# Performance work log

Measured on AMD Instinct MI355X. Metric: run time of the kernel, lower is better.

## Reference

```python
import jax, jax.numpy as jnp
import numpy as np

N, IN_DIM, OUT_DIM, HEADS = 2048, 512, 512, 8
HEAD_DIM = OUT_DIM // HEADS
NEG_SLOPE = 0.2


def setup_inputs() -> dict:
    key = jax.random.key(0)
    k1, k2, k3, k4 = jax.random.split(key, 4)
    x = jax.random.normal(k1, (N, IN_DIM), dtype=jnp.float32)
    adj = jax.random.randint(k2, (N, N), 0, 2, dtype=jnp.int32)
    W = jax.random.normal(k3, (IN_DIM, OUT_DIM), dtype=jnp.float32) * 0.02
    a = jax.random.normal(k4, (2 * HEAD_DIM,), dtype=jnp.float32) * 0.02
    return {"x": x, "adj": adj, "W": W, "a": a}


def reference(x, adj, W, a):
    # Wh: (N, H, Dh)
    Wh = (x @ W).reshape(N, HEADS, HEAD_DIM)
    # a . concat(Wh_i, Wh_j) == (Wh_i . a_src) + (Wh_j . a_dst) -- exact decomposition,
    # avoids materializing the (N, N, H, 2*Dh) concat tensor.
    a_src, a_dst = a[:HEAD_DIM], a[HEAD_DIM:]
    s_i = jnp.einsum('nhd,d->nh', Wh, a_src)  # contribution of dest node i
    s_j = jnp.einsum('nhd,d->nh', Wh, a_dst)  # contribution of source node j
    e = jax.nn.leaky_relu(s_i[:, None, :] + s_j[None, :, :], negative_slope=NEG_SLOPE)  # (N, N, H)
    mask = (adj > 0)[:, :, None]
    e = jnp.where(mask, e, jnp.float32(-jnp.inf))
    alpha = jax.nn.softmax(e, axis=1)  # softmax over source nodes j
    # out[i,h,:] = sum_j alpha[i,j,h] * Wh[j,h,:]   (dropout is identity at eval)
    out = jnp.einsum('ijh,jhd->ihd', alpha, Wh)
    return out.reshape(N, OUT_DIM)
```

## Files before the change

### kernel.cpp

```cpp
#include <hip/hip_runtime.h>
#include <hip/hip_bf16.h>

#define NN 2048
#define KD 512
#define ODIM 512
#define NHEAD 8
#define HD 64
#define NEG 0.2f

typedef float f32x4 __attribute__((ext_vector_type(4)));
typedef short bf16x8 __attribute__((ext_vector_type(8)));
typedef short bf16x4 __attribute__((ext_vector_type(4)));
typedef unsigned long long u64;
typedef unsigned int u32;

__device__ __forceinline__ short tob(float f) {
  __hip_bfloat16 h = __float2bfloat16(f);
  return *reinterpret_cast<short*>(&h);
}

__device__ __forceinline__ void gl_lds16(const void* g, void* l) {
  __builtin_amdgcn_global_load_lds(
      (const __attribute__((address_space(1))) u32*)g,
      (__attribute__((address_space(3))) u32*)l, 16, 0, 0);
}

__global__ __launch_bounds__(256) void prep(const float* __restrict__ W,
                                            const int* __restrict__ adj,
                                            __hip_bfloat16* __restrict__ WTb,
                                            unsigned short* __restrict__ bits) {
  const int b = blockIdx.x;
  const int t = threadIdx.x;
  if (b >= 64) {
    const int T = (b - 64) * 256 + t;
    const int row = T >> 7, g = T & 127;
    const int* p = adj + (size_t)row * NN + g * 16;
    u32 m = 0;
#pragma unroll
    for (int q = 0; q < 4; ++q) {
      const int4 v = *(const int4*)&p[q * 4];
      m |= (v.x > 0 ? 1u : 0u) << (q * 4);
      m |= (v.y > 0 ? 2u : 0u) << (q * 4);
      m |= (v.z > 0 ? 4u : 0u) << (q * 4);
      m |= (v.w > 0 ? 8u : 0u) << (q * 4);
    }
    bits[T] = (unsigned short)m;
    return;
  }
  __shared__ float tile[64][68];
  const int k0 = (b & 7) * 64, od0 = (b >> 3) * 64;
#pragma unroll
  for (int r = 0; r < 4; ++r) {
    const int flat = r * 256 + t;
    const int kk = flat >> 4, oq = (flat & 15) * 4;
    const float4 v = *(const float4*)&W[(size_t)(k0 + kk) * ODIM + od0 + oq];
    tile[kk][oq] = v.x;
    tile[kk][oq + 1] = v.y;
    tile[kk][oq + 2] = v.z;
    tile[kk][oq + 3] = v.w;
  }
  __syncthreads();
#pragma unroll
  for (int r = 0; r < 2; ++r) {
    const int flat = r * 256 + t;
    const int od = flat >> 3, kq = (flat & 7) * 8;
    bf16x8 o;
#pragma unroll
    for (int u = 0; u < 8; ++u) o[u] = tob(tile[kq + u][od]);
    *(bf16x8*)&WTb[(size_t)(od0 + od) * KD + k0 + kq] = o;
  }
}

__global__ __launch_bounds__(256) void gemm_fused(
    const float* __restrict__ X, const __hip_bfloat16* __restrict__ WTb,
    const float* __restrict__ a, short* __restrict__ WhF,
    float2* __restrict__ esrcp, u32* __restrict__ edstp) {
  __shared__ short As[64][72];
  __shared__ short Bs[64][72];
  const int t = threadIdx.x;
  const int lane = t & 63, w = t >> 6;
  const int col = lane & 15, kgrp = lane >> 4;
  const int bm = blockIdx.x * 64;
  const int h = blockIdx.y;

  const int am = t >> 2, ak = (t & 3) * 16;
  const int bn = t >> 2, bk = (t & 3) * 16;

  float4 xa[4];
  bf16x8 wb[2];
#pragma unroll
  for (int q = 0; q < 4; ++q)
    xa[q] = *(const float4*)&X[(size_t)(bm + am) * KD + ak + q * 4];
#pragma unroll
  for (int q = 0; q < 2; ++q)
    wb[q] = *(const bf16x8*)&WTb[(size_t)(h * 64 + bn) * KD + bk + q * 8];

  f32x4 acc[4] = {};

  for (int k0 = 0; k0 < KD; k0 += 64) {
#pragma unroll
    for (int q = 0; q < 2; ++q) {
      bf16x8 o;
#pragma unroll
      for (int u = 0; u < 4; ++u) {
        o[u] = tob(((const float*)&xa[q * 2])[u]);
        o[u + 4] = tob(((const float*)&xa[q * 2 + 1])[u]);
      }
      *(bf16x8*)&As[am][ak + q * 8] = o;
      *(bf16x8*)&Bs[bn][bk + q * 8] = wb[q];
    }
    __syncthreads();
    if (k0 + 64 < KD) {
      const int k1 = k0 + 64;
#pragma unroll
      for (int q = 0; q < 4; ++q)
        xa[q] = *(const float4*)&X[(size_t)(bm + am) * KD + k1 + ak + q * 4];
#pragma unroll
      for (int q = 0; q < 2; ++q)
        wb[q] = *(const bf16x8*)&WTb[(size_t)(h * 64 + bn) * KD + k1 + bk + q * 8];
    }
#pragma unroll
    for (int ks = 0; ks < 2; ++ks) {
      const bf16x8 af = *(const bf16x8*)&As[w * 16 + col][ks * 32 + kgrp * 8];
#pragma unroll
      for (int nt = 0; nt < 4; ++nt) {
        const bf16x8 bf = *(const bf16x8*)&Bs[nt * 16 + col][ks * 32 + kgrp * 8];
        acc[nt] = __builtin_amdgcn_mfma_f32_16x16x32_bf16(af, bf, acc[nt], 0, 0, 0);
      }
    }
    __syncthreads();
  }

  float asv[4], adv[4];
#pragma unroll
  for (int nt = 0; nt < 4; ++nt) {
    asv[nt] = a[nt * 16 + col];
    adv[nt] = a[64 + nt * 16 + col];
  }
  float ps[4], pd[4];
#pragma unroll
  for (int r = 0; r < 4; ++r) {
    float s1 = 0.f, s2 = 0.f;
#pragma unroll
    for (int nt = 0; nt < 4; ++nt) {
      s1 += acc[nt][r] * asv[nt];
      s2 += acc[nt][r] * adv[nt];
    }
    ps[r] = s1;
    pd[r] = s2;
  }
#pragma unroll
  for (int off = 1; off <= 8; off <<= 1) {
#pragma unroll
    for (int r = 0; r < 4; ++r) {
      ps[r] += __shfl_xor(ps[r], off);
      pd[r] += __shfl_xor(pd[r], off);
    }
  }
  {
    const size_t tbase = ((size_t)h * 32 + blockIdx.x) * 4096;
    const int lp = ((w & 1) * 2 + (kgrp >> 1)) * 16 + col;
    const int u0 = (kgrp & 1) * 4;
    const int slot_ks = w >> 1;
#pragma unroll
    for (int nt = 0; nt < 4; ++nt) {
      bf16x4 o;
#pragma unroll
      for (int r = 0; r < 4; ++r) o[r] = tob(acc[nt][r]);
      *(bf16x4*)&WhF[tbase + (size_t)(nt * 2 + slot_ks) * 512 + lp * 8 + u0] = o;
    }
  }
  if (col == 0) {
    const int mbase = bm + w * 16 + kgrp * 4;
#pragma unroll
    for (int r = 0; r < 4; ++r) {
      const int n = mbase + r;
      esrcp[h * NN + n] = make_float2(__expf(ps[r]), __expf(NEG * ps[r]));
      const u32 lo = (u32)(unsigned short)tob(__expf(pd[r]));
      const u32 hi = (u32)(unsigned short)tob(__expf(NEG * pd[r]));
      edstp[h * NN + n] = (hi << 16) | lo;
    }
  }
}

__global__ __launch_bounds__(512) void attn_mfma(
    const short* __restrict__ WhF, const unsigned char* __restrict__ adjbits,
    const float2* __restrict__ esrcp, const u32* __restrict__ edstp,
    float* __restrict__ out) {
  extern __shared__ __align__(16) char smem[];
  short* stage = (short*)smem;
  float* red = (float*)smem;

  const int t = threadIdx.x;
  const int lane = t & 63;
  const int wid = t >> 6;
  const int jq = wid >> 1;
  const int mh = wid & 1;
  const int col = lane & 15, kgrp = lane >> 4;
  const int h = blockIdx.y;
  const int i0 = blockIdx.x * 64;
  const int ib = i0 + mh * 32;

  const float2 e0 = esrcp[h * NN + ib + col];
  const float2 e1 = esrcp[h * NN + ib + 16 + col];
  const float A0 = e0.x, C0 = e0.y, A1 = e1.x, C1 = e1.y;
  const unsigned char* ab0 = adjbits + (size_t)(ib + col) * (NN / 8);
  const unsigned char* ab1 = adjbits + (size_t)(ib + 16 + col) * (NN / 8);

  bf16x8 ones;
#pragma unroll
  for (int u = 0; u < 8; ++u) ones[u] = (short)0x3F80;

  f32x4 acc[2][4] = {};
  f32x4 accd[2] = {};

  const short* tb = WhF + ((size_t)h * 32 + jq * 8) * 4096;
  const int jb = jq * 512;
  short* st0 = stage + (size_t)jq * (2 * 8 * 512);

#pragma unroll
  for (int s = 0; s < 4; ++s) {
    const int slot = mh * 4 + s;
    gl_lds16(tb + slot * 512 + lane * 8, st0 + slot * 512);
  }
  uint4 bd0, bd1, bd2, bd3;
  u64 aw0, aw1;
  {
    const int jj0 = jb + kgrp * 8;
    bd0 = *(const uint4*)&edstp[h * NN + jj0];
    bd1 = *(const uint4*)&edstp[h * NN + jj0 + 4];
    bd2 = *(const uint4*)&edstp[h * NN + jj0 + 32];
    bd3 = *(const uint4*)&edstp[h * NN + jj0 + 36];
    aw0 = *(const u64*)(ab0 + (jb >> 3));
    aw1 = *(const u64*)(ab1 + (jb >> 3));
  }
  __syncthreads();

#pragma unroll
  for (int tt = 0; tt < 8; ++tt) {
    short* scur = st0 + (tt & 1) * (8 * 512);
    short* snxt = st0 + ((tt + 1) & 1) * (8 * 512);
    if (tt < 7) {
      const short* g = tb + (size_t)(tt + 1) * 4096;
#pragma unroll
      for (int s = 0; s < 4; ++s) {
        const int slot = mh * 4 + s;
        gl_lds16(g + slot * 512 + lane * 8, snxt + slot * 512);
      }
    }
    uint4 bn0, bn1, bn2, bn3;
    u64 an0 = 0, an1 = 0;
    if (tt < 7) {
      const int j1 = jb + (tt + 1) * 64;
      const int jj1 = j1 + kgrp * 8;
      bn0 = *(const uint4*)&edstp[h * NN + jj1];
      bn1 = *(const uint4*)&edstp[h * NN + jj1 + 4];
      bn2 = *(const uint4*)&edstp[h * NN + jj1 + 32];
      bn3 = *(const uint4*)&edstp[h * NN + jj1 + 36];
      an0 = *(const u64*)(ab0 + (j1 >> 3));
      an1 = *(const u64*)(ab1 + (j1 >> 3));
    }
    bf16x8 af0[2], af1[2];
#pragma unroll
    for (int ks = 0; ks < 2; ++ks) {
      const u32 mb0 = (u32)(aw0 >> ((ks * 4 + kgrp) * 8)) & 0xffu;
      const u32 mb1 = (u32)(aw1 >> ((ks * 4 + kgrp) * 8)) & 0xffu;
      const uint4 q0 = ks ? bd2 : bd0;
      const uint4 q1 = ks ? bd3 : bd1;
      const u32 uw[8] = {q0.x, q0.y, q0.z, q0.w, q1.x, q1.y, q1.z, q1.w};
#pragma unroll
      for (int u2 = 0; u2 < 8; ++u2) {
        const float B = __uint_as_float(uw[u2] << 16);
        const float D = __uint_as_float(uw[u2] & 0xffff0000u);
        float p0 = fmaxf(A0 * B, C0 * D);
        float p1 = fmaxf(A1 * B, C1 * D);
        p0 = ((mb0 >> u2) & 1u) ? p0 : 0.f;
        p1 = ((mb1 >> u2) & 1u) ? p1 : 0.f;
        af0[ks][u2] = tob(p0);
        af1[ks][u2] = tob(p1);
      }
    }
    accd[0] = __builtin_amdgcn_mfma_f32_16x16x32_bf16(af0[0], ones, accd[0], 0, 0, 0);
    accd[0] = __builtin_amdgcn_mfma_f32_16x16x32_bf16(af0[1], ones, accd[0], 0, 0, 0);
    accd[1] = __builtin_amdgcn_mfma_f32_16x16x32_bf16(af1[0], ones, accd[1], 0, 0, 0);
    accd[1] = __builtin_amdgcn_mfma_f32_16x16x32_bf16(af1[1], ones, accd[1], 0, 0, 0);
#pragma unroll
    for (int nt = 0; nt < 4; ++nt) {
      const bf16x8 b0 = *(const bf16x8*)&scur[(nt * 2 + 0) * 512 + lane * 8];
      const bf16x8 b1 = *(const bf16x8*)&scur[(nt * 2 + 1) * 512 + lane * 8];
      acc[0][nt] = __builtin_amdgcn_mfma_f32_16x16x32_bf16(af0[0], b0, acc[0][nt], 0, 0, 0);
      acc[1][nt] = __builtin_amdgcn_mfma_f32_16x16x32_bf16(af1[0], b0, acc[1][nt], 0, 0, 0);
      acc[0][nt] = __builtin_amdgcn_mfma_f32_16x16x32_bf16(af0[1], b1, acc[0][nt], 0, 0, 0);
      acc[1][nt] = __builtin_amdgcn_mfma_f32_16x16x32_bf16(af1[1], b1, acc[1][nt], 0, 0, 0);
    }
    __syncthreads();
    if (tt < 7) {
      bd0 = bn0; bd1 = bn1; bd2 = bn2; bd3 = bn3;
      aw0 = an0; aw1 = an1;
    }
  }

  float* rw = red + (size_t)(mh * 4 + jq) * 32 * 66;
#pragma unroll
  for (int mt = 0; mt < 2; ++mt) {
#pragma unroll
    for (int nt = 0; nt < 4; ++nt)
#pragma unroll
      for (int r = 0; r < 4; ++r)
        rw[(mt * 16 + kgrp * 4 + r) * 66 + nt * 16 + col] = acc[mt][nt][r];
    if (col == 0) {
#pragma unroll
      for (int r = 0; r < 4; ++r)
        rw[(mt * 16 + kgrp * 4 + r) * 66 + 64] = accd[mt][r];
    }
  }
  __syncthreads();

  const int d = t & 63, rl = t >> 6;
#pragma unroll
  for (int rr = 0; rr < 8; ++rr) {
    const int row = rr * 8 + rl;
    const int m2 = row >> 5, r32 = row & 31;
    const float* rb = red + (size_t)(m2 * 4) * 32 * 66;
    float v = 0.f, dd = 0.f;
#pragma unroll
    for (int q = 0; q < 4; ++q) {
      v += rb[(q * 32 + r32) * 66 + d];
      dd += rb[(q * 32 + r32) * 66 + 64];
    }
    out[(size_t)(i0 + row) * ODIM + h * HD + d] = v / dd;
  }
}

extern "C" void kernel_launch(void* const* d_in, const int* in_sizes, int n_in,
                              void* d_out, int out_size, void* d_ws,
                              size_t ws_size, hipStream_t stream) {
  const float* x = (const float*)d_in[0];
  const int* adj = (const int*)d_in[1];
  const float* W = (const float*)d_in[2];
  const float* a = (const float*)d_in[3];
  float* out = (float*)d_out;

  char* ws = (char*)d_ws;
  short* WhF = (short*)ws;
  __hip_bfloat16* WTb = (__hip_bfloat16*)(ws + (2 << 20));
  unsigned short* bits =
      (unsigned short*)(ws + (2 << 20) + (512 << 10));
  float2* esrcp = (float2*)(ws + (3 << 20));
  u32* edstp = (u32*)(ws + (3 << 20) + (128 << 10));

  prep<<<1088, 256, 0, stream>>>(W, adj, WTb, bits);
  gemm_fused<<<dim3(32, 8), 256, 0, stream>>>(x, WTb, a, WhF, esrcp, edstp);
  attn_mfma<<<dim3(32, 8), 512, 67584, stream>>>(
      WhF, (const unsigned char*)bits, esrcp, edstp, out);
}
```

Before: 36.72 us.

## Give each attention wave a private LDS pipeline and halve the row tile

The attention kernel moves from 512-thread blocks covering 64 destination rows to 256-thread blocks covering 32 rows, which doubles the grid to 512 blocks. Each wave now double-buffers its own slice of Wh in LDS and waits with an explicit vmcnt count instead of a block-wide __syncthreads every step. The goal is to remove barrier stalls and fill more CUs. In exchange, each Wh tile is fetched once per 32 rows rather than per 64, so global and LDS traffic for Wh roughly doubles.

New measurement: 36.18 us. No clear change (-1.5%).

```diff
diff --git a/kernel.cpp b/kernel.cpp
--- a/kernel.cpp
+++ b/kernel.cpp
@@ -183,29 +183,26 @@
   }
 }
 
-__global__ __launch_bounds__(512) void attn_mfma(
+__global__ __launch_bounds__(256) void attn_mfma(
     const short* __restrict__ WhF, const unsigned char* __restrict__ adjbits,
     const float2* __restrict__ esrcp, const u32* __restrict__ edstp,
     float* __restrict__ out) {
   extern __shared__ __align__(16) char smem[];
-  short* stage = (short*)smem;
-  float* red = (float*)smem;
-
   const int t = threadIdx.x;
   const int lane = t & 63;
-  const int wid = t >> 6;
-  const int jq = wid >> 1;
-  const int mh = wid & 1;
+  const int jq = t >> 6;
   const int col = lane & 15, kgrp = lane >> 4;
   const int h = blockIdx.y;
-  const int i0 = blockIdx.x * 64;
-  const int ib = i0 + mh * 32;
-
-  const float2 e0 = esrcp[h * NN + ib + col];
-  const float2 e1 = esrcp[h * NN + ib + 16 + col];
+  const int i0 = blockIdx.x * 32;
+
+  const short* tb = WhF + ((size_t)h * 32 + jq * 8) * 4096;
+  const int jb = jq * 512;
+
+  const float2 e0 = esrcp[h * NN + i0 + col];
+  const float2 e1 = esrcp[h * NN + i0 + 16 + col];
   const float A0 = e0.x, C0 = e0.y, A1 = e1.x, C1 = e1.y;
-  const unsigned char* ab0 = adjbits + (size_t)(ib + col) * (NN / 8);
-  const unsigned char* ab1 = adjbits + (size_t)(ib + 16 + col) * (NN / 8);
+  const unsigned char* ab0 = adjbits + (size_t)(i0 + col) * (NN / 8);
+  const unsigned char* ab1 = adjbits + (size_t)(i0 + 16 + col) * (NN / 8);
 
   bf16x8 ones;
 #pragma unroll
@@ -214,59 +211,52 @@
   f32x4 acc[2][4] = {};
   f32x4 accd[2] = {};
 
-  const short* tb = WhF + ((size_t)h * 32 + jq * 8) * 4096;
-  const int jb = jq * 512;
-  short* st0 = stage + (size_t)jq * (2 * 8 * 512);
-
-#pragma unroll
-  for (int s = 0; s < 4; ++s) {
-    const int slot = mh * 4 + s;
-    gl_lds16(tb + slot * 512 + lane * 8, st0 + slot * 512);
-  }
-  uint4 bd0, bd1, bd2, bd3;
-  u64 aw0, aw1;
+  uint4 bd[2][4];
+  u64 aw[2][2];
+
   {
+    short* sb = (short*)(smem + jq * 16384);
+#pragma unroll
+    for (int s = 0; s < 8; ++s) gl_lds16(tb + s * 512 + lane * 8, sb + s * 512);
     const int jj0 = jb + kgrp * 8;
-    bd0 = *(const uint4*)&edstp[h * NN + jj0];
-    bd1 = *(const uint4*)&edstp[h * NN + jj0 + 4];
-    bd2 = *(const uint4*)&edstp[h * NN + jj0 + 32];
-    bd3 = *(const uint4*)&edstp[h * NN + jj0 + 36];
-    aw0 = *(const u64*)(ab0 + (jb >> 3));
-    aw1 = *(const u64*)(ab1 + (jb >> 3));
-  }
-  __syncthreads();
+    bd[0][0] = *(const uint4*)&edstp[h * NN + jj0];
+    bd[0][1] = *(const uint4*)&edstp[h * NN + jj0 + 4];
+    bd[0][2] = *(const uint4*)&edstp[h * NN + jj0 + 32];
+    bd[0][3] = *(const uint4*)&edstp[h * NN + jj0 + 36];
+    aw[0][0] = *(const u64*)(ab0 + (jb >> 3));
+    aw[0][1] = *(const u64*)(ab1 + (jb >> 3));
+  }
 
 #pragma unroll
   for (int tt = 0; tt < 8; ++tt) {
-    short* scur = st0 + (tt & 1) * (8 * 512);
-    short* snxt = st0 + ((tt + 1) & 1) * (8 * 512);
+    const int cur = tt & 1, nxt = cur ^ 1;
     if (tt < 7) {
       const short* g = tb + (size_t)(tt + 1) * 4096;
-#pragma unroll
-      for (int s = 0; s < 4; ++s) {
-        const int slot = mh * 4 + s;
-        gl_lds16(g + slot * 512 + lane * 8, snxt + slot * 512);
-      }
-    }
-    uint4 bn0, bn1, bn2, bn3;
-    u64 an0 = 0, an1 = 0;
-    if (tt < 7) {
+      short* sb = (short*)(smem + jq * 16384 + nxt * 8192);
+#pragma unroll
+      for (int s = 0; s < 8; ++s)
+        gl_lds16(g + s * 512 + lane * 8, sb + s * 512);
       const int j1 = jb + (tt + 1) * 64;
       const int jj1 = j1 + kgrp * 8;
-      bn0 = *(const uint4*)&edstp[h * NN + jj1];
-      bn1 = *(const uint4*)&edstp[h * NN + jj1 + 4];
-      bn2 = *(const uint4*)&edstp[h * NN + jj1 + 32];
-      bn3 = *(const uint4*)&edstp[h * NN + jj1 + 36];
-      an0 = *(const u64*)(ab0 + (j1 >> 3));
-      an1 = *(const u64*)(ab1 + (j1 >> 3));
-    }
+      bd[nxt][0] = *(const uint4*)&edstp[h * NN + jj1];
+      bd[nxt][1] = *(const uint4*)&edstp[h * NN + jj1 + 4];
+      bd[nxt][2] = *(const uint4*)&edstp[h * NN + jj1 + 32];
+      bd[nxt][3] = *(const uint4*)&edstp[h * NN + jj1 + 36];
+      aw[nxt][0] = *(const u64*)(ab0 + (j1 >> 3));
+      aw[nxt][1] = *(const u64*)(ab1 + (j1 >> 3));
+      asm volatile("s_waitcnt vmcnt(14)" ::: "memory");
+    } else {
+      asm volatile("s_waitcnt vmcnt(0)" ::: "memory");
+    }
+    __builtin_amdgcn_sched_barrier(0);
+
     bf16x8 af0[2], af1[2];
 #pragma unroll
     for (int ks = 0; ks < 2; ++ks) {
-      const u32 mb0 = (u32)(aw0 >> ((ks * 4 + kgrp) * 8)) & 0xffu;
-      const u32 mb1 = (u32)(aw1 >> ((ks * 4 + kgrp) * 8)) & 0xffu;
-      const uint4 q0 = ks ? bd2 : bd0;
-      const uint4 q1 = ks ? bd3 : bd1;
+      const u32 mb0 = (u32)(aw[cur][0] >> ((ks * 4 + kgrp) * 8)) & 0xffu;
+      const u32 mb1 = (u32)(aw[cur][1] >> ((ks * 4 + kgrp) * 8)) & 0xffu;
+      const uint4 q0 = bd[cur][ks * 2];
+      const uint4 q1 = bd[cur][ks * 2 + 1];
       const u32 uw[8] = {q0.x, q0.y, q0.z, q0.w, q1.x, q1.y, q1.z, q1.w};
 #pragma unroll
       for (int u2 = 0; u2 < 8; ++u2) {
@@ -280,6 +270,8 @@
         af1[ks][u2] = tob(p1);
       }
     }
+
+    const short* scur = (const short*)(smem + jq * 16384 + cur * 8192);
     accd[0] = __builtin_amdgcn_mfma_f32_16x16x32_bf16(af0[0], ones, accd[0], 0, 0, 0);
     accd[0] = __builtin_amdgcn_mfma_f32_16x16x32_bf16(af0[1], ones, accd[0], 0, 0, 0);
     accd[1] = __builtin_amdgcn_mfma_f32_16x16x32_bf16(af1[0], ones, accd[1], 0, 0, 0);
@@ -293,14 +285,11 @@
       acc[0][nt] = __builtin_amdgcn_mfma_f32_16x16x32_bf16(af0[1], b1, acc[0][nt], 0, 0, 0);
       acc[1][nt] = __builtin_amdgcn_mfma_f32_16x16x32_bf16(af1[1], b1, acc[1][nt], 0, 0, 0);
     }
-    __syncthreads();
-    if (tt < 7) {
-      bd0 = bn0; bd1 = bn1; bd2 = bn2; bd3 = bn3;
-      aw0 = an0; aw1 = an1;
-    }
-  }
-
-  float* rw = red + (size_t)(mh * 4 + jq) * 32 * 66;
+  }
+
+  __syncthreads();
+  float* red = (float*)smem;
+  float* rw = red + (size_t)jq * 32 * 66;
 #pragma unroll
   for (int mt = 0; mt < 2; ++mt) {
 #pragma unroll
@@ -319,14 +308,12 @@
   const int d = t & 63, rl = t >> 6;
 #pragma unroll
   for (int rr = 0; rr < 8; ++rr) {
-    const int row = rr * 8 + rl;
-    const int m2 = row >> 5, r32 = row & 31;
-    const float* rb = red + (size_t)(m2 * 4) * 32 * 66;
+    const int row = rr * 4 + rl;
     float v = 0.f, dd = 0.f;
 #pragma unroll
     for (int q = 0; q < 4; ++q) {
-      v += rb[(q * 32 + r32) * 66 + d];
-      dd += rb[(q * 32 + r32) * 66 + 64];
+      v += red[((size_t)q * 32 + row) * 66 + d];
+      dd += red[((size_t)q * 32 + row) * 66 + 64];
     }
     out[(size_t)(i0 + row) * ODIM + h * HD + d] = v / dd;
   }
@@ -351,6 +338,6 @@
 
   prep<<<1088, 256, 0, stream>>>(W, adj, WTb, bits);
   gemm_fused<<<dim3(32, 8), 256, 0, stream>>>(x, WTb, a, WhF, esrcp, edstp);
-  attn_mfma<<<dim3(32, 8), 512, 67584, stream>>>(
+  attn_mfma<<<dim3(64, 8), 256, 65536, stream>>>(
       WhF, (const unsigned char*)bits, esrcp, edstp, out);
 }
```
